# Performance work log

Measured on AMD Instinct MI355X. Metric: run time of the kernel, lower is better.

Reference implementation:

```python
import jax, jax.numpy as jnp
import numpy as np

EPS = 1e-5

def _ln(x, w, b):
    mu = x.mean(-1, keepdims=True)
    var = ((x - mu) ** 2).mean(-1, keepdims=True)
    return (x - mu) * jax.lax.rsqrt(var + EPS) * w + b

def _shift(x):
    # ZeroPad2d((0,0,1,-1)): x_shifted[:, t] = x[:, t-1], zero at t=0
    return jnp.pad(x, ((0, 0), (1, 0), (0, 0)))[:, :-1]

def _time_mix(x, u, w, mk, mv, mr, Wk, Wv, Wr, Wo, bo):
    xs = _shift(x)
    k = (x * mk + xs * (1 - mk)) @ Wk.T            # [B,T,d]
    v = (x * mv + xs * (1 - mv)) @ Wv.T
    r = jax.nn.sigmoid(x * mr + xs * (1 - mr)) @ Wr.T
    B, T, d = x.shape

    def step(carry, kv):
        a, b = carry
        kt, vt = kv                                 # [B,d]
        q = jnp.maximum(u + kt, w)
        e1 = jnp.exp(-w - q)
        e2 = jnp.exp(u + kt - q)
        a = e1 * a + e2 * vt
        b = e1 * b + e2
        return (a, b), a / b

    a0 = jnp.zeros((B, d), x.dtype)
    b0 = jnp.zeros((B, d), x.dtype)
    _, wkv = jax.lax.scan(step, (a0, b0), (k.transpose(1, 0, 2), v.transpose(1, 0, 2)))
    wkv = wkv.transpose(1, 0, 2)                    # [B,T,d]
    return (wkv * r) @ Wo.T + bo

def _channel_mix(x, mk, mr, Wk, Wv, Wr):
    xs = _shift(x)
    k = jnp.square(jax.nn.relu((x * mk + xs * (1 - mk)) @ Wk.T))
    v = k @ Wv.T
    r = jax.nn.sigmoid((x * mr + xs * (1 - mr)) @ Wr.T)
    return r * v

def setup_inputs() -> dict:
    B, T, d = 8, 2048, 2048
    key = jax.random.key(0)
    ks = jax.random.split(key, 16)
    s = 0.02
    return {
        "x": jax.random.normal(ks[0], (B, T, d), jnp.float32),
        "ln1_w": jnp.ones((d,), jnp.float32),
        "ln1_b": jnp.zeros((d,), jnp.float32),
        "ln2_w": jnp.ones((d,), jnp.float32),
        "ln2_b": jnp.zeros((d,), jnp.float32),
        "tm_u": 0.1 * jax.random.normal(ks[1], (d,), jnp.float32),
        "tm_w": jnp.ones((d,), jnp.float32) + 0.1 * jax.random.normal(ks[2], (d,), jnp.float32),
        "tm_mix_k": jax.random.uniform(ks[3], (d,), jnp.float32),
        "tm_mix_v": jax.random.uniform(ks[4], (d,), jnp.float32),
        "tm_mix_r": jax.random.uniform(ks[5], (d,), jnp.float32),
        "tm_Wk": s * jax.random.normal(ks[6], (d, d), jnp.float32),
        "tm_Wv": s * jax.random.normal(ks[7], (d, d), jnp.float32),
        "tm_Wr": s * jax.random.normal(ks[8], (d, d), jnp.float32),
        "tm_Wo": s * jax.random.normal(ks[9], (d, d), jnp.float32),
        "tm_bo": jnp.zeros((d,), jnp.float32),
        "cm_mix_k": jax.random.uniform(ks[10], (d,), jnp.float32),
        "cm_mix_r": jax.random.uniform(ks[11], (d,), jnp.float32),
        "cm_Wk": s * jax.random.normal(ks[12], (d, d), jnp.float32),
        "cm_Wv": s * jax.random.normal(ks[13], (d, d), jnp.float32),
        "cm_Wr": s * jax.random.normal(ks[14], (d, d), jnp.float32),
    }

def reference(x, ln1_w, ln1_b, ln2_w, ln2_b, tm_u, tm_w, tm_mix_k, tm_mix_v, tm_mix_r, tm_Wk, tm_Wv, tm_Wr, tm_Wo, tm_bo, cm_mix_k, cm_mix_r, cm_Wk, cm_Wv, cm_Wr):
    att = _time_mix(_ln(x, ln1_w, ln1_b), tm_u, tm_w, tm_mix_k, tm_mix_v, tm_mix_r, tm_Wk, tm_Wv, tm_Wr, tm_Wo, tm_bo)
    x = x + att
    ffn = _channel_mix(_ln(x, ln2_w, ln2_b), cm_mix_k, cm_mix_r, cm_Wk, cm_Wv, cm_Wr)
    return x + ffn
```

## Files before the change

kernel.cpp:

```cpp
#include <hip/hip_runtime.h>
#include <hip/hip_bf16.h>
#include <stdint.h>

typedef __bf16 bf16x8 __attribute__((ext_vector_type(8)));
typedef float floatx4 __attribute__((ext_vector_type(4)));

__device__ __forceinline__ float bf2f(__hip_bfloat16 v) { return __bfloat162float(v); }
__device__ __forceinline__ __hip_bfloat16 f2bf(float v) { return __float2bfloat16(v); }

#define WKV_CH 64

__global__ __launch_bounds__(256) void k_f2bf(const float* __restrict__ in,
                                              __hip_bfloat16* __restrict__ out, int n) {
    int i = blockIdx.x * 256 + threadIdx.x;
    if (i < n) out[i] = f2bf(in[i]);
}

__global__ __launch_bounds__(256) void k_ln(const float* __restrict__ x,
                                            const float* __restrict__ w,
                                            const float* __restrict__ b,
                                            __hip_bfloat16* __restrict__ out, int d) {
    __shared__ float red[8];
    const size_t row = blockIdx.x;
    const float* xr = x + row * (size_t)d;
    float s = 0.f, ss = 0.f;
    for (int i = threadIdx.x; i < d; i += 256) {
        float v = xr[i];
        s += v; ss += v * v;
    }
    for (int off = 32; off > 0; off >>= 1) {
        s  += __shfl_down(s,  off, 64);
        ss += __shfl_down(ss, off, 64);
    }
    int wv = threadIdx.x >> 6, ln = threadIdx.x & 63;
    if (ln == 0) { red[wv] = s; red[4 + wv] = ss; }
    __syncthreads();
    s  = red[0] + red[1] + red[2] + red[3];
    ss = red[4] + red[5] + red[6] + red[7];
    float mu  = s / d;
    float var = ss / d - mu * mu;
    float rs  = rsqrtf(var + 1e-5f);
    __hip_bfloat16* orow = out + row * (size_t)d;
    for (int i = threadIdx.x; i < d; i += 256) {
        orow[i] = f2bf((xr[i] - mu) * rs * w[i] + b[i]);
    }
}

__global__ __launch_bounds__(256) void k_tmix(const __hip_bfloat16* __restrict__ xln,
    const float* __restrict__ mk, const float* __restrict__ mv, const float* __restrict__ mr,
    __hip_bfloat16* __restrict__ xk, __hip_bfloat16* __restrict__ xv, __hip_bfloat16* __restrict__ xr,
    int T, int d) {
    const int c = blockIdx.x * 256 + threadIdx.x;
    const size_t row = blockIdx.y;
    const int t = (int)(row % (size_t)T);
    const size_t idx = row * (size_t)d + c;
    float xc = bf2f(xln[idx]);
    float xs = t ? bf2f(xln[idx - d]) : 0.f;
    float a = mk[c];
    xk[idx] = f2bf(xc * a + xs * (1.f - a));
    float bq = mv[c];
    xv[idx] = f2bf(xc * bq + xs * (1.f - bq));
    float rm = mr[c];
    float pre = xc * rm + xs * (1.f - rm);
    xr[idx] = f2bf(1.f / (1.f + __expf(-pre)));
}

__global__ __launch_bounds__(256) void k_cmix(const __hip_bfloat16* __restrict__ xln,
    const float* __restrict__ mk, const float* __restrict__ mr,
    __hip_bfloat16* __restrict__ xk, __hip_bfloat16* __restrict__ xr,
    int T, int d) {
    const int c = blockIdx.x * 256 + threadIdx.x;
    const size_t row = blockIdx.y;
    const int t = (int)(row % (size_t)T);
    const size_t idx = row * (size_t)d + c;
    float xc = bf2f(xln[idx]);
    float xs = t ? bf2f(xln[idx - d]) : 0.f;
    float a = mk[c];
    xk[idx] = f2bf(xc * a + xs * (1.f - a));
    float rm = mr[c];
    xr[idx] = f2bf(xc * rm + xs * (1.f - rm));
}

__global__ __launch_bounds__(256) void k_wkv_p1(const __hip_bfloat16* __restrict__ k,
    const __hip_bfloat16* __restrict__ v,
    const float* __restrict__ u, const float* __restrict__ w,
    float* __restrict__ Ac, float* __restrict__ Bc, float* __restrict__ Pc,
    int T, int d, int nch) {
    const int idx = blockIdx.x * 256 + threadIdx.x;
    const int c = idx & (d - 1);
    const int rest = idx / d;
    const int j = rest & (nch - 1);
    const int b = rest / nch;
    const float uc = u[c], wc = w[c];
    float aa = 0.f, bb = 0.f, P = 0.f;
    const size_t base = ((size_t)b * T + (size_t)j * WKV_CH) * d + c;
#pragma unroll 4
    for (int t = 0; t < WKV_CH; ++t) {
        float kt = bf2f(k[base + (size_t)t * d]);
        float vt = bf2f(v[base + (size_t)t * d]);
        float q  = fmaxf(uc + kt, wc);
        float e1 = __expf(-wc - q);
        float e2 = __expf(uc + kt - q);
        aa = e1 * aa + e2 * vt;
        bb = e1 * bb + e2;
        P += wc + q;
    }
    const size_t s = ((size_t)b * nch + j) * d + c;
    Ac[s] = aa; Bc[s] = bb; Pc[s] = P;
}

__global__ __launch_bounds__(256) void k_wkv_p2(const float* __restrict__ Ac,
    const float* __restrict__ Bc, const float* __restrict__ Pc,
    float* __restrict__ Ain, float* __restrict__ Bin, int d, int nch) {
    const int idx = blockIdx.x * 256 + threadIdx.x;
    const int c = idx & (d - 1);
    const int b = idx / d;
    float a = 0.f, bbs = 0.f;
    for (int j = 0; j < nch; ++j) {
        const size_t s = ((size_t)b * nch + j) * d + c;
        Ain[s] = a; Bin[s] = bbs;
        float p = __expf(-Pc[s]);
        a   = p * a   + Ac[s];
        bbs = p * bbs + Bc[s];
    }
}

__global__ __launch_bounds__(256) void k_wkv_p3(const __hip_bfloat16* __restrict__ k,
    const __hip_bfloat16* v,
    const __hip_bfloat16* __restrict__ r,
    const float* __restrict__ u, const float* __restrict__ w,
    const float* __restrict__ Ain, const float* __restrict__ Bin,
    __hip_bfloat16* out, int T, int d, int nch) {
    const int idx = blockIdx.x * 256 + threadIdx.x;
    const int c = idx & (d - 1);
    const int rest = idx / d;
    const int j = rest & (nch - 1);
    const int b = rest / nch;
    const float uc = u[c], wc = w[c];
    const size_t s = ((size_t)b * nch + j) * d + c;
    float aa = Ain[s], bb = Bin[s];
    const size_t base = ((size_t)b * T + (size_t)j * WKV_CH) * d + c;
#pragma unroll 4
    for (int t = 0; t < WKV_CH; ++t) {
        float kt = bf2f(k[base + (size_t)t * d]);
        float vt = bf2f(v[base + (size_t)t * d]);
        float rt = bf2f(r[base + (size_t)t * d]);
        float q  = fmaxf(uc + kt, wc);
        float e1 = __expf(-wc - q);
        float e2 = __expf(uc + kt - q);
        aa = e1 * aa + e2 * vt;
        bb = e1 * bb + e2;
        out[base + (size_t)t * d] = f2bf((aa / bb) * rt);
    }
}

#define GM_BF16  0
#define GM_ADDX  1
#define GM_SIG   2
#define GM_RELU2 3
#define GM_FINAL 4

#define REGLDS(reg) ((unsigned)((reg) == 0 ? 0u : (reg) == 1 ? 32768u : (reg) == 2 ? 16384u : 49152u))
#define SBAR() __builtin_amdgcn_sched_barrier(0)

template<int MODE>
__global__ __launch_bounds__(512, 2)
void gemm_bt(const __hip_bfloat16* __restrict__ A,
             const __hip_bfloat16* __restrict__ B,
             void* __restrict__ outv,
             const float* __restrict__ auxf,
             const float* __restrict__ bias,
             const __hip_bfloat16* __restrict__ auxb,
             int N, int K) {
    __shared__ char smem[131072];
    const int tid  = threadIdx.x;
    const int lane = tid & 63;
    const int wave = tid >> 6;
    const int wm = wave >> 2;
    const int wn = wave & 3;
    const int NT = K >> 6;
    const size_t Kb = (size_t)K * 2;

    const int gx = gridDim.x, gy = gridDim.y;
    const int nwg = gx * gy;
    int bid = blockIdx.y * gx + blockIdx.x;
    int L = bid;
    if ((nwg & 7) == 0) {
        const int cpx = nwg >> 3;
        L = (bid & 7) * cpx + (bid >> 3);
    }
    const int bn = (L % gx) * 256;
    const int bm = (L / gx) * 256;

    const int rh0 = tid >> 3;
    const int kc8 = ((tid & 7) ^ (rh0 & 7)) << 3;
    const size_t offA = ((size_t)(bm + rh0) * K + kc8) * 2;
    const size_t offB = ((size_t)(bn + rh0) * K + kc8) * 2;
    const unsigned waveBase = (unsigned)(wave * 64);

#define STAGE(tau, reg) do {                                                        \
    int _tt = (tau);                                                                \
    if (_tt < NT) {                                                                 \
        const char* _gp = ((reg) & 1) ? (const char*)B : (const char*)A;            \
        size_t _go = (((reg) & 1) ? offB : offA)                                    \
                   + (((reg) >= 2) ? (size_t)128 * Kb : 0) + (size_t)_tt * 128;     \
        unsigned _lb = ((unsigned)(_tt & 1) << 16) + REGLDS(reg);                   \
        _Pragma("unroll")                                                           \
        for (int _q = 0; _q < 2; ++_q) {                                            \
            __builtin_amdgcn_global_load_lds(                                       \
                (__attribute__((address_space(1))) void*)(_gp + _go + (size_t)_q * 64 * Kb), \
                (__attribute__((address_space(3))) void*)(smem + _lb + (unsigned)(_q * 512 + waveBase) * 16), \
                16, 0, 0);                                                          \
        }                                                                           \
    }                                                                               \
} while (0)

    const int lane15 = lane & 15;
    const int laneHi = lane >> 4;
    const int chunk0 = ((laneHi)     ^ (lane & 7)) << 4;
    const int chunk1 = ((laneHi + 4) ^ (lane & 7)) << 4;
    const int aLane = (wm * 64 + lane15) * 128;
    const int bLane = 32768 + (wn * 32 + lane15) * 128;

    floatx4 acc00[4][2] = {}, acc01[4][2] = {}, acc11[4][2] = {}, acc10[4][2] = {};
    bf16x8 a[4][2], b0[2][2], b1[2][2];

    STAGE(0, 0); STAGE(0, 1); STAGE(0, 2); STAGE(0, 3);
    STAGE(1, 0); STAGE(1, 1); STAGE(1, 2);
    asm volatile("s_waitcnt vmcnt(6)" ::: "memory");
    SBAR(); __builtin_amdgcn_s_barrier(); SBAR();

#pragma unroll 2
    for (int t = 0; t < NT; ++t) {
        const char* sA = smem + ((t & 1) << 16) + aLane;
        const char* sB = smem + ((t & 1) << 16) + bLane;

#pragma unroll
        for (int i = 0; i < 4; ++i) {
            a[i][0] = *(const bf16x8*)(sA + i * 2048 + chunk0);
            a[i][1] = *(const bf16x8*)(sA + i * 2048 + chunk1);
        }
#pragma unroll
        for (int j = 0; j < 2; ++j) {
            b0[j][0] = *(const bf16x8*)(sB + j * 2048 + chunk0);
            b0[j][1] = *(const bf16x8*)(sB + j * 2048 + chunk1);
        }
        STAGE(t + 1, 3);
        SBAR(); __builtin_amdgcn_s_barrier(); SBAR();
        __builtin_amdgcn_s_setprio(1);
#pragma unroll
        for (int i = 0; i < 4; ++i)
#pragma unroll
            for (int j = 0; j < 2; ++j) {
                acc00[i][j] = __builtin_amdgcn_mfma_f32_16x16x32_bf16(a[i][0], b0[j][0], acc00[i][j], 0, 0, 0);
                acc00[i][j] = __builtin_amdgcn_mfma_f32_16x16x32_bf16(a[i][1], b0[j][1], acc00[i][j], 0, 0, 0);
            }
        __builtin_amdgcn_s_setprio(0);
        SBAR(); __builtin_amdgcn_s_barrier(); SBAR();

#pragma unroll
        for (int j = 0; j < 2; ++j) {
            b1[j][0] = *(const bf16x8*)(sB + 16384 + j * 2048 + chunk0);
            b1[j][1] = *(const bf16x8*)(sB + 16384 + j * 2048 + chunk1);
        }
        STAGE(t + 2, 0);
        SBAR(); __builtin_amdgcn_s_barrier(); SBAR();
        __builtin_amdgcn_s_setprio(1);
#pragma unroll
        for (int i = 0; i < 4; ++i)
#pragma unroll
            for (int j = 0; j < 2; ++j) {
                acc01[i][j] = __builtin_amdgcn_mfma_f32_16x16x32_bf16(a[i][0], b1[j][0], acc01[i][j], 0, 0, 0);
                acc01[i][j] = __builtin_amdgcn_mfma_f32_16x16x32_bf16(a[i][1], b1[j][1], acc01[i][j], 0, 0, 0);
            }
        __builtin_amdgcn_s_setprio(0);
        SBAR(); __builtin_amdgcn_s_barrier(); SBAR();

#pragma unroll
        for (int i = 0; i < 4; ++i) {
            a[i][0] = *(const bf16x8*)(sA + 16384 + i * 2048 + chunk0);
            a[i][1] = *(const bf16x8*)(sA + 16384 + i * 2048 + chunk1);
        }
        STAGE(t + 2, 1);
        SBAR(); __builtin_amdgcn_s_barrier(); SBAR();
        __builtin_amdgcn_s_setprio(1);
#pragma unroll
        for (int i = 0; i < 4; ++i)
#pragma unroll
            for (int j = 0; j < 2; ++j) {
                acc11[i][j] = __builtin_amdgcn_mfma_f32_16x16x32_bf16(a[i][0], b1[j][0], acc11[i][j], 0, 0, 0);
                acc11[i][j] = __builtin_amdgcn_mfma_f32_16x16x32_bf16(a[i][1], b1[j][1], acc11[i][j], 0, 0, 0);
            }
        __builtin_amdgcn_s_setprio(0);
        SBAR(); __builtin_amdgcn_s_barrier(); SBAR();

        STAGE(t + 2, 2);
        SBAR(); __builtin_amdgcn_s_barrier(); SBAR();
        __builtin_amdgcn_s_setprio(1);
#pragma unroll
        for (int i = 0; i < 4; ++i)
#pragma unroll
            for (int j = 0; j < 2; ++j) {
                acc10[i][j] = __builtin_amdgcn_mfma_f32_16x16x32_bf16(a[i][0], b0[j][0], acc10[i][j], 0, 0, 0);
                acc10[i][j] = __builtin_amdgcn_mfma_f32_16x16x32_bf16(a[i][1], b0[j][1], acc10[i][j], 0, 0, 0);
            }
        __builtin_amdgcn_s_setprio(0);
        SBAR();
        if (t + 2 < NT) {
            asm volatile("s_waitcnt vmcnt(6)" ::: "memory");
        } else {
            asm volatile("s_waitcnt vmcnt(0)" ::: "memory");
        }
        __builtin_amdgcn_s_barrier(); SBAR();
    }
#undef STAGE

    const int erow = bm + wm * 64 + (laneHi << 2);
    const int ecol = bn + wn * 32 + lane15;
#define EPI(ACC, MH, NH)                                                            \
    _Pragma("unroll")                                                               \
    for (int i = 0; i < 4; ++i) {                                                   \
        _Pragma("unroll")                                                           \
        for (int jf = 0; jf < 2; ++jf) {                                            \
            const int c = ecol + (NH) * 128 + jf * 16;                              \
            _Pragma("unroll")                                                       \
            for (int j = 0; j < 4; ++j) {                                           \
                const int r = erow + (MH) * 128 + i * 16 + j;                       \
                const size_t idx = (size_t)r * N + c;                               \
                const float val = ACC[i][jf][j];                                    \
                if (MODE == GM_BF16) {                                              \
                    ((__hip_bfloat16*)outv)[idx] = f2bf(val);                       \
                } else if (MODE == GM_ADDX) {                                       \
                    ((float*)outv)[idx] = auxf[idx] + bias[c] + val;                \
                } else if (MODE == GM_SIG) {                                        \
                    ((__hip_bfloat16*)outv)[idx] = f2bf(1.f / (1.f + __expf(-val))); \
                } else if (MODE == GM_RELU2) {                                      \
                    float tp = fmaxf(val, 0.f);                                     \
                    ((__hip_bfloat16*)outv)[idx] = f2bf(tp * tp);                   \
                } else {                                                            \
                    float* o = (float*)outv;                                        \
                    o[idx] = o[idx] + bf2f(auxb[idx]) * val;                        \
                }                                                                   \
            }                                                                       \
        }                                                                           \
    }
    EPI(acc00, 0, 0)
    EPI(acc01, 0, 1)
    EPI(acc11, 1, 1)
    EPI(acc10, 1, 0)
#undef EPI
}

extern "C" void kernel_launch(void* const* d_in, const int* in_sizes, int n_in,
                              void* d_out, int out_size, void* d_ws, size_t ws_size,
                              hipStream_t stream) {
    const float* x      = (const float*)d_in[0];
    const float* ln1_w  = (const float*)d_in[1];
    const float* ln1_b  = (const float*)d_in[2];
    const float* ln2_w  = (const float*)d_in[3];
    const float* ln2_b  = (const float*)d_in[4];
    const float* tm_u   = (const float*)d_in[5];
    const float* tm_w   = (const float*)d_in[6];
    const float* tm_mk  = (const float*)d_in[7];
    const float* tm_mv  = (const float*)d_in[8];
    const float* tm_mr  = (const float*)d_in[9];
    const float* tm_bo  = (const float*)d_in[14];
    const float* cm_mk  = (const float*)d_in[15];
    const float* cm_mr  = (const float*)d_in[16];

    const int D = in_sizes[1];
    const int Mrows = in_sizes[0] / D;
    const int T = 2048;
    const int Bb = Mrows / T;
    const size_t dd = (size_t)D * D;
    const size_t md = (size_t)Mrows * D;
    const int nch = T / WKV_CH;

    __hip_bfloat16* W = (__hip_bfloat16*)d_ws;
    __hip_bfloat16* buf[7];
    for (int i = 0; i < 7; ++i) buf[i] = W + 7 * dd + (size_t)i * md;

    float* S = (float*)buf[0];
    const size_t cs = (size_t)Bb * nch * D;
    float* Ac  = S;
    float* Bc  = S + cs;
    float* Pc  = S + 2 * cs;
    float* Ain = S + 3 * cs;
    float* Bin = S + 4 * cs;

    const int widx[7] = {10, 11, 12, 13, 17, 18, 19};
    for (int i = 0; i < 7; ++i)
        k_f2bf<<<(int)(dd / 256), 256, 0, stream>>>((const float*)d_in[widx[i]], W + (size_t)i * dd, (int)dd);

    k_ln<<<Mrows, 256, 0, stream>>>(x, ln1_w, ln1_b, buf[0], D);
    k_tmix<<<dim3(D / 256, Mrows), 256, 0, stream>>>(buf[0], tm_mk, tm_mv, tm_mr,
                                                     buf[1], buf[2], buf[3], T, D);
    dim3 gg(D / 256, Mrows / 256);
    gemm_bt<GM_BF16><<<gg, 512, 0, stream>>>(buf[1], W + 0 * dd, buf[4], nullptr, nullptr, nullptr, D, D);
    gemm_bt<GM_BF16><<<gg, 512, 0, stream>>>(buf[2], W + 1 * dd, buf[5], nullptr, nullptr, nullptr, D, D);
    gemm_bt<GM_BF16><<<gg, 512, 0, stream>>>(buf[3], W + 2 * dd, buf[6], nullptr, nullptr, nullptr, D, D);

    k_wkv_p1<<<(Bb * D * nch) / 256, 256, 0, stream>>>(buf[4], buf[5], tm_u, tm_w,
                                                       Ac, Bc, Pc, T, D, nch);
    k_wkv_p2<<<(Bb * D) / 256, 256, 0, stream>>>(Ac, Bc, Pc, Ain, Bin, D, nch);
    k_wkv_p3<<<(Bb * D * nch) / 256, 256, 0, stream>>>(buf[4], buf[5], buf[6], tm_u, tm_w,
                                                       Ain, Bin, buf[5], T, D, nch);

    gemm_bt<GM_ADDX><<<gg, 512, 0, stream>>>(buf[5], W + 3 * dd, d_out, x, tm_bo, nullptr, D, D);
    k_ln<<<Mrows, 256, 0, stream>>>((const float*)d_out, ln2_w, ln2_b, buf[0], D);
    k_cmix<<<dim3(D / 256, Mrows), 256, 0, stream>>>(buf[0], cm_mk, cm_mr, buf[1], buf[2], T, D);
    gemm_bt<GM_SIG><<<gg, 512, 0, stream>>>(buf[2], W + 6 * dd, buf[3], nullptr, nullptr, nullptr, D, D);
    gemm_bt<GM_RELU2><<<gg, 512, 0, stream>>>(buf[1], W + 4 * dd, buf[6], nullptr, nullptr, nullptr, D, D);
    gemm_bt<GM_FINAL><<<gg, 512, 0, stream>>>(buf[6], W + 5 * dd, d_out, nullptr, nullptr, buf[3], D, D);
}
```

Measured before the change: 1.720 ms.

## Double-buffer GEMM register fragments to prefetch next K tile during MFMA

Restructures the bf16 GEMM main loop so that LDS fragment reads for the next K-tile (A low half and B low half) are issued during the current tile's last MFMA phase. Separate aLo/aHi and alternating bP/bQ register buffers are used, and the loop is unrolled by two to swap roles. The prologue now stages all four regions of tile 1 and preloads the first fragments. The aim is to hide LDS read latency behind MFMA work. In exchange it adds live vector registers, which under the 512-thread, 2-block launch bound could raise register pressure or cause spills.

```diff
diff --git a/kernel.cpp b/kernel.cpp
--- a/kernel.cpp
+++ b/kernel.cpp
@@ -162,6 +162,7 @@
 
 #define REGLDS(reg) ((unsigned)((reg) == 0 ? 0u : (reg) == 1 ? 32768u : (reg) == 2 ? 16384u : 49152u))
 #define SBAR() __builtin_amdgcn_sched_barrier(0)
+#define LGKM0() asm volatile("s_waitcnt lgkmcnt(0)" ::: "memory")
 
 template<int MODE>
 __global__ __launch_bounds__(512, 2)
@@ -222,97 +223,87 @@
     const int aLane = (wm * 64 + lane15) * 128;
     const int bLane = 32768 + (wn * 32 + lane15) * 128;
 
+#define RDA(dst, base, off) do {                                                     \
+    _Pragma("unroll")                                                                \
+    for (int _i = 0; _i < 4; ++_i) {                                                 \
+        dst[_i][0] = *(const bf16x8*)((base) + (off) + _i * 2048 + chunk0);          \
+        dst[_i][1] = *(const bf16x8*)((base) + (off) + _i * 2048 + chunk1);          \
+    }                                                                                \
+} while (0)
+
+#define RDB(dst, base, off) do {                                                     \
+    _Pragma("unroll")                                                                \
+    for (int _j = 0; _j < 2; ++_j) {                                                 \
+        dst[_j][0] = *(const bf16x8*)((base) + (off) + _j * 2048 + chunk0);          \
+        dst[_j][1] = *(const bf16x8*)((base) + (off) + _j * 2048 + chunk1);          \
+    }                                                                                \
+} while (0)
+
+#define MM(ACC, AF, BF) do {                                                         \
+    __builtin_amdgcn_s_setprio(1);                                                   \
+    _Pragma("unroll")                                                                \
+    for (int _i = 0; _i < 4; ++_i)                                                   \
+        _Pragma("unroll")                                                            \
+        for (int _j = 0; _j < 2; ++_j) {                                             \
+            ACC[_i][_j] = __builtin_amdgcn_mfma_f32_16x16x32_bf16(AF[_i][0], BF[_j][0], ACC[_i][_j], 0, 0, 0); \
+            ACC[_i][_j] = __builtin_amdgcn_mfma_f32_16x16x32_bf16(AF[_i][1], BF[_j][1], ACC[_i][_j], 0, 0, 0); \
+        }                                                                            \
+    __builtin_amdgcn_s_setprio(0);                                                   \
+} while (0)
+
     floatx4 acc00[4][2] = {}, acc01[4][2] = {}, acc11[4][2] = {}, acc10[4][2] = {};
-    bf16x8 a[4][2], b0[2][2], b1[2][2];
+    bf16x8 aLo[4][2], aHi[4][2], bP[2][2], bQ[2][2];
 
     STAGE(0, 0); STAGE(0, 1); STAGE(0, 2); STAGE(0, 3);
-    STAGE(1, 0); STAGE(1, 1); STAGE(1, 2);
-    asm volatile("s_waitcnt vmcnt(6)" ::: "memory");
+    STAGE(1, 0); STAGE(1, 1); STAGE(1, 2); STAGE(1, 3);
+    asm volatile("s_waitcnt vmcnt(8)" ::: "memory");
     SBAR(); __builtin_amdgcn_s_barrier(); SBAR();
-
-#pragma unroll 2
-    for (int t = 0; t < NT; ++t) {
-        const char* sA = smem + ((t & 1) << 16) + aLane;
-        const char* sB = smem + ((t & 1) << 16) + bLane;
-
-#pragma unroll
-        for (int i = 0; i < 4; ++i) {
-            a[i][0] = *(const bf16x8*)(sA + i * 2048 + chunk0);
-            a[i][1] = *(const bf16x8*)(sA + i * 2048 + chunk1);
-        }
-#pragma unroll
-        for (int j = 0; j < 2; ++j) {
-            b0[j][0] = *(const bf16x8*)(sB + j * 2048 + chunk0);
-            b0[j][1] = *(const bf16x8*)(sB + j * 2048 + chunk1);
-        }
-        STAGE(t + 1, 3);
-        SBAR(); __builtin_amdgcn_s_barrier(); SBAR();
-        __builtin_amdgcn_s_setprio(1);
-#pragma unroll
-        for (int i = 0; i < 4; ++i)
-#pragma unroll
-            for (int j = 0; j < 2; ++j) {
-                acc00[i][j] = __builtin_amdgcn_mfma_f32_16x16x32_bf16(a[i][0], b0[j][0], acc00[i][j], 0, 0, 0);
-                acc00[i][j] = __builtin_amdgcn_mfma_f32_16x16x32_bf16(a[i][1], b0[j][1], acc00[i][j], 0, 0, 0);
-            }
-        __builtin_amdgcn_s_setprio(0);
-        SBAR(); __builtin_amdgcn_s_barrier(); SBAR();
-
-#pragma unroll
-        for (int j = 0; j < 2; ++j) {
-            b1[j][0] = *(const bf16x8*)(sB + 16384 + j * 2048 + chunk0);
-            b1[j][1] = *(const bf16x8*)(sB + 16384 + j * 2048 + chunk1);
-        }
-        STAGE(t + 2, 0);
-        SBAR(); __builtin_amdgcn_s_barrier(); SBAR();
-        __builtin_amdgcn_s_setprio(1);
-#pragma unroll
-        for (int i = 0; i < 4; ++i)
-#pragma unroll
-            for (int j = 0; j < 2; ++j) {
-                acc01[i][j] = __builtin_amdgcn_mfma_f32_16x16x32_bf16(a[i][0], b1[j][0], acc01[i][j], 0, 0, 0);
-                acc01[i][j] = __builtin_amdgcn_mfma_f32_16x16x32_bf16(a[i][1], b1[j][1], acc01[i][j], 0, 0, 0);
-            }
-        __builtin_amdgcn_s_setprio(0);
-        SBAR(); __builtin_amdgcn_s_barrier(); SBAR();
-
-#pragma unroll
-        for (int i = 0; i < 4; ++i) {
-            a[i][0] = *(const bf16x8*)(sA + 16384 + i * 2048 + chunk0);
-            a[i][1] = *(const bf16x8*)(sA + 16384 + i * 2048 + chunk1);
-        }
-        STAGE(t + 2, 1);
-        SBAR(); __builtin_amdgcn_s_barrier(); SBAR();
-        __builtin_amdgcn_s_setprio(1);
-#pragma unroll
-        for (int i = 0; i < 4; ++i)
-#pragma unroll
-            for (int j = 0; j < 2; ++j) {
-                acc11[i][j] = __builtin_amdgcn_mfma_f32_16x16x32_bf16(a[i][0], b1[j][0], acc11[i][j], 0, 0, 0);
-                acc11[i][j] = __builtin_amdgcn_mfma_f32_16x16x32_bf16(a[i][1], b1[j][1], acc11[i][j], 0, 0, 0);
-            }
-        __builtin_amdgcn_s_setprio(0);
-        SBAR(); __builtin_amdgcn_s_barrier(); SBAR();
-
-        STAGE(t + 2, 2);
-        SBAR(); __builtin_amdgcn_s_barrier(); SBAR();
-        __builtin_amdgcn_s_setprio(1);
-#pragma unroll
-        for (int i = 0; i < 4; ++i)
-#pragma unroll
-            for (int j = 0; j < 2; ++j) {
-                acc10[i][j] = __builtin_amdgcn_mfma_f32_16x16x32_bf16(a[i][0], b0[j][0], acc10[i][j], 0, 0, 0);
-                acc10[i][j] = __builtin_amdgcn_mfma_f32_16x16x32_bf16(a[i][1], b0[j][1], acc10[i][j], 0, 0, 0);
-            }
-        __builtin_amdgcn_s_setprio(0);
-        SBAR();
-        if (t + 2 < NT) {
-            asm volatile("s_waitcnt vmcnt(6)" ::: "memory");
-        } else {
-            asm volatile("s_waitcnt vmcnt(0)" ::: "memory");
-        }
-        __builtin_amdgcn_s_barrier(); SBAR();
-    }
+    RDA(aLo, smem + aLane, 0);
+    RDB(bP, smem + bLane, 0);
+    LGKM0();
+    SBAR(); __builtin_amdgcn_s_barrier(); SBAR();
+
+#define TILE(T, BU, BW) do {                                                         \
+    const char* sA  = smem + (((T) & 1) << 16) + aLane;                              \
+    const char* sB  = smem + (((T) & 1) << 16) + bLane;                              \
+    const char* sAn = smem + ((((T) + 1) & 1) << 16) + aLane;                        \
+    const char* sBn = smem + ((((T) + 1) & 1) << 16) + bLane;                        \
+                      \
+    RDB(BW, sB, 16384);                                                              \
+    STAGE((T) + 2, 0);                                                               \
+    SBAR(); __builtin_amdgcn_s_barrier(); SBAR();                                    \
+    MM(acc00, aLo, BU);                                                              \
+    LGKM0();                                                                         \
+    SBAR(); __builtin_amdgcn_s_barrier(); SBAR();                                    \
+                        \
+    RDA(aHi, sA, 16384);                                                             \
+    STAGE((T) + 2, 1);                                                               \
+    SBAR(); __builtin_amdgcn_s_barrier(); SBAR();                                    \
+    MM(acc01, aLo, BW);                                                              \
+    LGKM0();                                                                         \
+    SBAR(); __builtin_amdgcn_s_barrier(); SBAR();                                    \
+             \
+    STAGE((T) + 2, 2);                                                               \
+    SBAR(); __builtin_amdgcn_s_barrier(); SBAR();                                    \
+    MM(acc11, aHi, BW);                                                              \
+    if ((T) + 2 < NT) { asm volatile("s_waitcnt vmcnt(6)" ::: "memory"); }           \
+    else              { asm volatile("s_waitcnt vmcnt(0)" ::: "memory"); }           \
+    SBAR(); __builtin_amdgcn_s_barrier(); SBAR();                                    \
+      \
+    RDA(aLo, sAn, 0);                                                                \
+    RDB(BW, sBn, 0);                                                                 \
+    STAGE((T) + 2, 3);                                                               \
+    SBAR(); __builtin_amdgcn_s_barrier(); SBAR();                                    \
+    MM(acc10, aHi, BU);                                                              \
+    LGKM0();                                                                         \
+    SBAR(); __builtin_amdgcn_s_barrier(); SBAR();                                    \
+} while (0)
+
+    for (int t = 0; t < NT; t += 2) {
+        TILE(t, bP, bQ);
+        TILE(t + 1, bQ, bP);
+    }
+#undef TILE
 #undef STAGE
 
     const int erow = bm + wm * 64 + (laneHi << 2);
```

After: 2.362 ms. 1.37x slower.
